# Kernel optimization log

Measured on AMD Instinct MI355X. Metric: run time of the kernel, lower is better.

Reference implementation:

```python
import jax, jax.numpy as jnp
import numpy as np

HEAD_DIM = 64
NUM_FEATURES = 256


def _sample_orf(head_dim, num_features, seed=0):
    """Orthogonal random features with chi(d)-norm row scaling (FAVOR+)."""
    rng = np.random.RandomState(seed)
    blocks = []
    while len(blocks) * head_dim < num_features:
        G = rng.randn(head_dim, head_dim).astype(np.float32)
        Q, _ = np.linalg.qr(G)
        norms = np.linalg.norm(rng.randn(head_dim, head_dim).astype(np.float32), axis=1)
        blocks.append(np.diag(norms) @ Q.T)
    return np.concatenate(blocks, axis=0)[:num_features].astype(np.float32)


def _phi(x, omega, is_query):
    """FAVOR+ positive feature map with max-subtraction stabilization."""
    m = omega.shape[0]
    proj = jnp.einsum('bhnd,md->bhnm', x, omega)          # [B,H,N,M]
    norm = 0.5 * jnp.sum(x * x, axis=-1, keepdims=True)    # [B,H,N,1]
    log_phi = proj - norm
    if is_query:
        log_phi = log_phi - jnp.max(log_phi, axis=-1, keepdims=True)
    else:
        log_phi = log_phi - jnp.max(log_phi)
    return jnp.exp(log_phi) / np.float32(np.sqrt(m)) + 1e-4


def _causal_scan(phi_q, phi_k, v):
    """Causal linear-attention recurrence via lax.scan. States: S[B,H,M,D], z[B,H,M]."""
    B, H, N, M = phi_q.shape
    D = v.shape[-1]
    # seq-first for scan: [N,B,H,*]
    pq = jnp.moveaxis(phi_q, 2, 0)
    pk = jnp.moveaxis(phi_k, 2, 0)
    vt = jnp.moveaxis(v, 2, 0)

    S0 = jnp.zeros((B, H, M, D), dtype=phi_q.dtype)
    z0 = jnp.zeros((B, H, M), dtype=phi_q.dtype)

    def step(carry, xs):
        S, z = carry
        pq_i, pk_i, v_i = xs  # [B,H,M], [B,H,M], [B,H,D]
        S = S + pk_i[..., :, None] * v_i[..., None, :]
        z = z + pk_i
        num = jnp.einsum('bhm,bhmd->bhd', pq_i, S)
        den = jnp.sum(pq_i * z, axis=-1, keepdims=True) + 1e-6
        return (S, z), num / den

    _, out = jax.lax.scan(step, (S0, z0), (pq, pk, vt))  # out: [N,B,H,D]
    return jnp.moveaxis(out, 0, 2)


def setup_inputs() -> dict:
    key = jax.random.key(0)
    k1, k2, k3 = jax.random.split(key, 3)
    B, H, N, D = 2, 16, 4096, HEAD_DIM
    q = jax.random.normal(k1, (B, H, N, D), dtype=jnp.float32)
    k = jax.random.normal(k2, (B, H, N, D), dtype=jnp.float32)
    v = jax.random.normal(k3, (B, H, N, D), dtype=jnp.float32)
    omega = jnp.asarray(_sample_orf(HEAD_DIM, NUM_FEATURES))
    return {"q": q, "k": k, "v": v, "omega": omega}


def reference(q, k, v, omega):
    scale = q.shape[-1] ** (-0.25)
    phi_q = _phi(q * scale, omega, is_query=True)
    phi_k = _phi(k * scale, omega, is_query=False)
    # q_len == kv_len -> causal scan branch (matches original forward)
    out = _causal_scan(phi_q.astype(jnp.float32), phi_k.astype(jnp.float32),
                       v.astype(jnp.float32))
    return out.astype(q.dtype)
```

## Files before the change

kernel.cpp:

```cpp
#include <hip/hip_runtime.h>
#include <cstddef>

#define BH    32
#define NSEQ  4096
#define MFEAT 256
#define CHUNK 128
#define NCH   32
#define SROW  65
#define SPITCH (SROW*256)

#define SCALE 0.35355339059327373f

typedef unsigned int uint_t;
typedef _Float16 half_t;
typedef __attribute__((ext_vector_type(8))) _Float16 half8;
typedef __attribute__((ext_vector_type(4))) float f32x4;

__device__ __forceinline__ f32x4 mfma16(half8 a, half8 b, f32x4 c) {
  return __builtin_amdgcn_mfma_f32_16x16x32_f16(a, b, c, 0, 0, 0);
}
__device__ __forceinline__ uint_t enc_f(float x) {
  uint_t u = __float_as_uint(x);
  return (u & 0x80000000u) ? ~u : (u | 0x80000000u);
}
__device__ __forceinline__ float dec_f(uint_t u) {
  u = (u & 0x80000000u) ? (u ^ 0x80000000u) : ~u;
  return __uint_as_float(u);
}
__device__ __forceinline__ half8 cvt_h8(float4 a, float4 b) {
  half8 h;
  h[0] = (half_t)a.x; h[1] = (half_t)a.y; h[2] = (half_t)a.z; h[3] = (half_t)a.w;
  h[4] = (half_t)b.x; h[5] = (half_t)b.y; h[6] = (half_t)b.z; h[7] = (half_t)b.w;
  return h;
}

__global__ void k_init(uint_t* kmax) { *kmax = enc_f(-__builtin_inff()); }

__global__ __launch_bounds__(256, 2) void k_maxes3(
    const float* __restrict__ q, const float* __restrict__ kx,
    const float* __restrict__ omega, uint_t* __restrict__ kmax,
    half_t* __restrict__ phiQ, half_t* __restrict__ kh,
    float* __restrict__ hnKg)
{
  __shared__ half_t Wl[256 * 72];
  __shared__ float nrm[64];
  __shared__ float red[4];

  const int tid = threadIdx.x;
  const int lane = tid & 63;
  const int w = tid >> 6;
  const int lc = lane & 15, rg = lane >> 4, koff = rg * 8;
  const size_t rowbase = (size_t)blockIdx.x * 64;

  for (int l = tid; l < 4096; l += 256) {
    int m = l >> 4, d4 = (l & 15) * 4;
    float4 o = *(const float4*)(omega + m * 64 + d4);
    half_t* p = &Wl[m * 72 + d4];
    p[0] = (half_t)o.x; p[1] = (half_t)o.y; p[2] = (half_t)o.z; p[3] = (half_t)o.w;
  }
  half8 aq[2], akf[2];
  {
    const float* qp = q + (rowbase + w * 16 + lc) * 64 + koff;
    const float* kp = kx + (rowbase + w * 16 + lc) * 64 + koff;
    float pn = 0.f;
    #pragma unroll
    for (int ks = 0; ks < 2; ks++) {
      float4 a = *(const float4*)(qp + ks * 32);
      float4 b = *(const float4*)(qp + ks * 32 + 4);
      a.x *= SCALE; a.y *= SCALE; a.z *= SCALE; a.w *= SCALE;
      b.x *= SCALE; b.y *= SCALE; b.z *= SCALE; b.w *= SCALE;
      aq[ks] = cvt_h8(a, b);
      float4 c = *(const float4*)(kp + ks * 32);
      float4 d = *(const float4*)(kp + ks * 32 + 4);
      c.x *= SCALE; c.y *= SCALE; c.z *= SCALE; c.w *= SCALE;
      d.x *= SCALE; d.y *= SCALE; d.z *= SCALE; d.w *= SCALE;
      pn += c.x * c.x + c.y * c.y + c.z * c.z + c.w * c.w
          + d.x * d.x + d.y * d.y + d.z * d.z + d.w * d.w;
      akf[ks] = cvt_h8(c, d);
    }
    #pragma unroll
    for (int ks = 0; ks < 2; ks++)
      *(half8*)(kh + (rowbase + w * 16 + lc) * 64 + ks * 32 + koff) = akf[ks];
    pn += __shfl_xor(pn, 16, 64);
    pn += __shfl_xor(pn, 32, 64);
    if (rg == 0) {
      nrm[w * 16 + lc] = 0.5f * pn;
      hnKg[rowbase + w * 16 + lc] = 0.5f * pn;
    }
  }
  __syncthreads();

  {
    f32x4 acc[16];
    #pragma unroll
    for (int ct = 0; ct < 16; ct++) acc[ct] = (f32x4){0.f, 0.f, 0.f, 0.f};
    #pragma unroll
    for (int ks = 0; ks < 2; ks++)
      #pragma unroll
      for (int ct = 0; ct < 16; ct++) {
        half8 b = *(const half8*)&Wl[(ct * 16 + lc) * 72 + ks * 32 + koff];
        acc[ct] = mfma16(akf[ks], b, acc[ct]);
      }
    float hn[4];
    #pragma unroll
    for (int r = 0; r < 4; r++) hn[r] = nrm[w * 16 + rg * 4 + r];
    float bm = -3.4e38f;
    #pragma unroll
    for (int ct = 0; ct < 16; ct++)
      #pragma unroll
      for (int r = 0; r < 4; r++) bm = fmaxf(bm, acc[ct][r] - hn[r]);
    #pragma unroll
    for (int off = 1; off < 64; off <<= 1) bm = fmaxf(bm, __shfl_xor(bm, off, 64));
    if (lane == 0) red[w] = bm;
  }

  f32x4 acc[16];
  #pragma unroll
  for (int ct = 0; ct < 16; ct++) acc[ct] = (f32x4){0.f, 0.f, 0.f, 0.f};
  #pragma unroll
  for (int ks = 0; ks < 2; ks++)
    #pragma unroll
    for (int ct = 0; ct < 16; ct++) {
      half8 b = *(const half8*)&Wl[(ct * 16 + lc) * 72 + ks * 32 + koff];
      acc[ct] = mfma16(aq[ks], b, acc[ct]);
    }
  float rowm[4];
  #pragma unroll
  for (int r = 0; r < 4; r++) {
    float m0 = -3.4e38f;
    #pragma unroll
    for (int ct = 0; ct < 16; ct++) m0 = fmaxf(m0, acc[ct][r]);
    m0 = fmaxf(m0, __shfl_xor(m0, 1, 64));
    m0 = fmaxf(m0, __shfl_xor(m0, 2, 64));
    m0 = fmaxf(m0, __shfl_xor(m0, 4, 64));
    m0 = fmaxf(m0, __shfl_xor(m0, 8, 64));
    rowm[r] = m0;
  }
  #pragma unroll
  for (int ct = 0; ct < 16; ct++)
    #pragma unroll
    for (int r = 0; r < 4; r++)
      acc[ct][r] = __expf(acc[ct][r] - rowm[r]) * 0.0625f + 1e-4f;

  __syncthreads();
  if (tid == 0)
    atomicMax(kmax, enc_f(fmaxf(fmaxf(red[0], red[1]), fmaxf(red[2], red[3]))));

  half_t* st = Wl;
  #pragma unroll
  for (int ct = 0; ct < 16; ct++)
    #pragma unroll
    for (int r = 0; r < 4; r++)
      st[(w * 16 + rg * 4 + r) * 264 + ct * 16 + lc] = (half_t)acc[ct][r];
  __syncthreads();
  #pragma unroll
  for (int e = 0; e < 8; e++) {
    int l = tid + e * 256;
    int row = l >> 5, c = (l & 31) * 8;
    *(half8*)(phiQ + (rowbase + row) * 256 + c) = *(const half8*)&st[row * 264 + c];
  }
}

__global__ __launch_bounds__(256, 2) void k_state3(
    const half_t* __restrict__ kh, const float* __restrict__ v,
    const float* __restrict__ omega, const float* __restrict__ hnKg,
    const uint_t* __restrict__ kmax, half_t* __restrict__ spA,
    half_t* __restrict__ phiKg)
{
  __shared__ half_t WP[256 * 72];
  __shared__ half_t vt[80 * 136];

  const int tid = threadIdx.x;
  const int lane = tid & 63;
  const int w = tid >> 6;
  const int lc = lane & 15, rg = lane >> 4, koff = rg * 8;
  const int wr = w * 32;
  const int blk = blockIdx.x;
  const size_t nbase = (size_t)(blk >> 5) * NSEQ + (size_t)(blk & 31) * CHUNK;
  const float gmaxv = dec_f(*kmax);

  for (int l = tid; l < 4096; l += 256) {
    int m = l >> 4, d4 = (l & 15) * 4;
    float4 o = *(const float4*)(omega + m * 64 + d4);
    half_t* p = &WP[m * 72 + d4];
    p[0] = (half_t)o.x; p[1] = (half_t)o.y; p[2] = (half_t)o.z; p[3] = (half_t)o.w;
  }
  for (int l = tid; l < 2048; l += 256) {
    int j = l >> 4, dq = (l & 15) * 4;
    float4 vv = *(const float4*)(v + (nbase + j) * 64 + dq);
    vt[(dq + 0) * 136 + j] = (half_t)vv.x;
    vt[(dq + 1) * 136 + j] = (half_t)vv.y;
    vt[(dq + 2) * 136 + j] = (half_t)vv.z;
    vt[(dq + 3) * 136 + j] = (half_t)vv.w;
  }
  if (tid < 128) vt[64 * 136 + tid] = (half_t)1.0f;

  half8 ak[2][2];
  float hnr[2][4];
  #pragma unroll
  for (int rt = 0; rt < 2; rt++) {
    const half_t* kp = kh + (nbase + wr + rt * 16 + lc) * 64 + koff;
    ak[rt][0] = *(const half8*)(kp);
    ak[rt][1] = *(const half8*)(kp + 32);
    #pragma unroll
    for (int r = 0; r < 4; r++)
      hnr[rt][r] = hnKg[nbase + wr + rt * 16 + rg * 4 + r];
  }
  __syncthreads();

  f32x4 accP[2][16];
  #pragma unroll
  for (int rt = 0; rt < 2; rt++)
    #pragma unroll
    for (int ct = 0; ct < 16; ct++) accP[rt][ct] = (f32x4){0.f, 0.f, 0.f, 0.f};
  #pragma unroll
  for (int ks = 0; ks < 2; ks++)
    #pragma unroll
    for (int ct = 0; ct < 16; ct++) {
      half8 b = *(const half8*)&WP[(ct * 16 + lc) * 72 + ks * 32 + koff];
      accP[0][ct] = mfma16(ak[0][ks], b, accP[0][ct]);
      accP[1][ct] = mfma16(ak[1][ks], b, accP[1][ct]);
    }
  #pragma unroll
  for (int rt = 0; rt < 2; rt++)
    #pragma unroll
    for (int ct = 0; ct < 16; ct++)
      #pragma unroll
      for (int r = 0; r < 4; r++)
        accP[rt][ct][r] = __expf(accP[rt][ct][r] - hnr[rt][r] - gmaxv) * 0.0625f + 1e-4f;

  half_t* pkT = WP;
  #pragma unroll
  for (int h = 0; h < 2; h++) {
    __syncthreads();
    #pragma unroll
    for (int rt = 0; rt < 2; rt++)
      #pragma unroll
      for (int c8 = 0; c8 < 8; c8++) {
        int ct = h * 8 + c8;
        #pragma unroll
        for (int r = 0; r < 4; r++)
          pkT[(c8 * 16 + lc) * 144 + wr + rt * 16 + rg * 4 + r] = (half_t)accP[rt][ct][r];
      }
    __syncthreads();
    f32x4 acc2[5][2];
    #pragma unroll
    for (int rt = 0; rt < 5; rt++) {
      acc2[rt][0] = (f32x4){0.f, 0.f, 0.f, 0.f};
      acc2[rt][1] = (f32x4){0.f, 0.f, 0.f, 0.f};
    }
    #pragma unroll
    for (int ks = 0; ks < 4; ks++) {
      half8 b0 = *(const half8*)&pkT[((2 * w + 0) * 16 + lc) * 144 + ks * 32 + koff];
      half8 b1 = *(const half8*)&pkT[((2 * w + 1) * 16 + lc) * 144 + ks * 32 + koff];
      #pragma unroll
      for (int rt = 0; rt < 5; rt++) {
        half8 a = *(const half8*)&vt[(rt * 16 + lc) * 136 + ks * 32 + koff];
        acc2[rt][0] = mfma16(a, b0, acc2[rt][0]);
        acc2[rt][1] = mfma16(a, b1, acc2[rt][1]);
      }
    }
    #pragma unroll
    for (int rt = 0; rt < 5; rt++)
      #pragma unroll
      for (int c2 = 0; c2 < 2; c2++)
        #pragma unroll
        for (int r = 0; r < 4; r++) {
          int row = rt * 16 + rg * 4 + r;
          if (row < SROW)
            spA[(size_t)blk * SPITCH + row * 256 + h * 128 + (2 * w + c2) * 16 + lc] =
                (half_t)acc2[rt][c2][r];
        }
  }

  half_t* PhS = WP;
  #pragma unroll
  for (int hh = 0; hh < 2; hh++) {
    __syncthreads();
    #pragma unroll
    for (int rt = 0; rt < 2; rt++)
      #pragma unroll
      for (int c8 = 0; c8 < 8; c8++)
        #pragma unroll
        for (int r = 0; r < 4; r++)
          PhS[(wr + rt * 16 + rg * 4 + r) * 136 + c8 * 16 + lc] =
              (half_t)accP[rt][hh * 8 + c8][r];
    __syncthreads();
    #pragma unroll
    for (int e = 0; e < 8; e++) {
      int l = tid + e * 256;
      int j = l >> 4, c8b = (l & 15) * 8;
      *(half8*)(phiKg + (nbase + j) * 256 + hh * 128 + c8b) =
          *(const half8*)&PhS[j * 136 + c8b];
    }
  }
}

__global__ __launch_bounds__(256) void k_prefix(
    const uint_t* __restrict__ spA, uint_t* __restrict__ spB)
{
  int r = blockIdx.x * 256 + threadIdx.x;
  if (r >= SPITCH / 2) return;
  int bh = blockIdx.y;
  const uint_t* src = spA + (size_t)bh * NCH * (SPITCH / 2) + r;
  uint_t* dst = spB + (size_t)bh * NCH * (SPITCH / 2) + r;
  float r0 = 0.f, r1 = 0.f;
  for (int c = 0; c < NCH; c++) {
    union { uint_t u; half_t h[2]; } cv, ov;
    cv.u = src[(size_t)c * (SPITCH / 2)];
    ov.h[0] = (half_t)r0; ov.h[1] = (half_t)r1;
    dst[(size_t)c * (SPITCH / 2)] = ov.u;
    r0 += (float)cv.h[0];
    r1 += (float)cv.h[1];
  }
}

__global__ __launch_bounds__(512) void k_attn8(
    const half_t* __restrict__ phiQ, const half_t* __restrict__ phiK,
    const float* __restrict__ v, const half_t* __restrict__ spB,
    float* __restrict__ out)
{
  __shared__ half_t sm[18432];
  half_t* PQ  = sm;
  half_t* SST = sm + 8192;
  half_t* AS  = sm;
  half_t* VT  = sm + 8192;

  const int tid = threadIdx.x;
  const int lane = tid & 63;
  const int w = tid >> 6;
  const int lc = lane & 15, rg = lane >> 4, koff = rg * 8;
  const int blk = blockIdx.x;
  const size_t nbase = (size_t)(blk >> 5) * NSEQ + (size_t)(blk & 31) * CHUNK;
  const half_t* spb = spB + (size_t)blk * SPITCH;
  const int swz = (lc & 7) << 3;

  f32x4 accA[8], accO[5];
  #pragma unroll
  for (int it = 0; it < 8; it++) accA[it] = (f32x4){0.f, 0.f, 0.f, 0.f};
  #pragma unroll
  for (int cs = 0; cs < 5; cs++) accO[cs] = (f32x4){0.f, 0.f, 0.f, 0.f};

  for (int mt = 0; mt < 4; mt++) {
    if (mt) __syncthreads();
    #pragma unroll
    for (int e = 0; e < 2; e++) {
      int l = tid + e * 512;
      int ro = l >> 3, c8 = (l & 7) * 8;
      *(half8*)&PQ[ro * 64 + (c8 ^ ((ro & 7) << 3))] =
          *(const half8*)(phiQ + (nbase + ro) * 256 + mt * 64 + c8);
    }
    { int ro = tid >> 3, c8 = (tid & 7) * 8;
      if (tid < 520)
        *(half8*)&SST[ro * 64 + (c8 ^ ((ro & 7) << 3))] =
            *(const half8*)(spb + ro * 256 + mt * 64 + c8); }
    if (tid < 8) { int l = tid + 512; int ro = l >> 3, c8 = (l & 7) * 8;
      *(half8*)&SST[ro * 64 + (c8 ^ ((ro & 7) << 3))] =
          *(const half8*)(spb + ro * 256 + mt * 64 + c8); }
    half8 af0 = *(const half8*)(phiK + (nbase + w * 16 + lc) * 256 + mt * 64 + koff);
    half8 af1 = *(const half8*)(phiK + (nbase + w * 16 + lc) * 256 + mt * 64 + 32 + koff);
    __syncthreads();
    #pragma unroll
    for (int ks2 = 0; ks2 < 64; ks2 += 32) {
      half8 a = ks2 ? af1 : af0;
      int sA = (ks2 + koff) ^ swz;
      half8 bO = *(const half8*)&PQ[(w * 16 + lc) * 64 + sA];
      #pragma unroll
      for (int it = 0; it < 8; it++) {
        half8 b = *(const half8*)&PQ[(it * 16 + lc) * 64 + sA];
        accA[it] = mfma16(a, b, accA[it]);
      }
      #pragma unroll
      for (int cs = 0; cs < 5; cs++) {
        half8 as_ = *(const half8*)&SST[(cs * 16 + lc) * 64 + sA];
        accO[cs] = mfma16(as_, bO, accO[cs]);
      }
    }
  }
  __syncthreads();

  #pragma unroll
  for (int e = 0; e < 4; e++) {
    int l = tid + e * 512;
    int j = l >> 4, dq = (l & 15) * 4;
    float4 vv = *(const float4*)(v + (nbase + j) * 64 + dq);
    VT[(dq + 0) * 128 + (j ^ (((dq + 0) & 7) << 3))] = (half_t)vv.x;
    VT[(dq + 1) * 128 + (j ^ (((dq + 1) & 7) << 3))] = (half_t)vv.y;
    VT[(dq + 2) * 128 + (j ^ (((dq + 2) & 7) << 3))] = (half_t)vv.z;
    VT[(dq + 3) * 128 + (j ^ (((dq + 3) & 7) << 3))] = (half_t)vv.w;
  }
  if (tid < 128) VT[64 * 128 + tid] = (half_t)1.0f;

  #pragma unroll
  for (int h = 0; h < 2; h++) {
    if ((w >> 2) == h) {
      #pragma unroll
      for (int it = 0; it < 8; it++) {
        int i = it * 16 + lc;
        #pragma unroll
        for (int r = 0; r < 4; r++) {
          int j = w * 16 + rg * 4 + r;
          float val = (j <= i) ? accA[it][r] : 0.f;
          AS[i * 64 + ((j - h * 64) ^ ((i & 7) << 3))] = (half_t)val;
        }
      }
    }
    __syncthreads();
    #pragma unroll
    for (int ks2 = 0; ks2 < 64; ks2 += 32) {
      int sj = (ks2 + koff) ^ swz;
      half8 b = *(const half8*)&AS[(w * 16 + lc) * 64 + sj];
      #pragma unroll
      for (int cs = 0; cs < 5; cs++) {
        half8 a = *(const half8*)&VT[(cs * 16 + lc) * 128 + ((h * 64 + ks2 + koff) ^ swz)];
        accO[cs] = mfma16(a, b, accO[cs]);
      }
    }
    __syncthreads();
  }

  float den = __shfl(accO[4][0], lane & 15, 64) + 1e-6f;
  float inv = 1.0f / den;
  float* OS = (float*)sm;
  #pragma unroll
  for (int cs = 0; cs < 4; cs++)
    #pragma unroll
    for (int r = 0; r < 4; r++)
      OS[(w * 16 + lc) * 68 + cs * 16 + rg * 4 + r] = accO[cs][r] * inv;
  __syncthreads();
  #pragma unroll
  for (int e = 0; e < 4; e++) {
    int l = tid + e * 512;
    int row = l >> 4, c4 = (l & 15) * 4;
    *(float4*)(out + (nbase + row) * 64 + c4) = *(const float4*)&OS[row * 68 + c4];
  }
}

extern "C" void kernel_launch(void* const* d_in, const int* in_sizes, int n_in,
                              void* d_out, int out_size, void* d_ws, size_t ws_size,
                              hipStream_t stream) {
  const float* q = (const float*)d_in[0];
  const float* k = (const float*)d_in[1];
  const float* v = (const float*)d_in[2];
  const float* omega = (const float*)d_in[3];
  float* out = (float*)d_out;
  char* ws = (char*)d_ws;

  float*  hnKg = (float*)(ws + 0);
  half_t* kh   = (half_t*)(ws + 524288);
  half_t* spB  = (half_t*)(ws + 524288);
  half_t* phiQ = (half_t*)(ws + 34603008);
  half_t* phiK = (half_t*)(ws + 101711872);
  half_t* spA  = (half_t*)(ws + 168820736);
  uint_t* kmax = (uint_t*)(ws + 202899456);

  k_init<<<1, 1, 0, stream>>>(kmax);
  k_maxes3<<<2048, 256, 0, stream>>>(q, k, omega, kmax, phiQ, kh, hnKg);
  k_state3<<<1024, 256, 0, stream>>>(kh, v, omega, hnKg, kmax, spA, phiK);
  k_prefix<<<dim3(33, 32), 256, 0, stream>>>((const uint_t*)spA, (uint_t*)spB);
  k_attn8<<<1024, 512, 0, stream>>>(phiQ, phiK, v, spB, out);
}
```

Before: 167.2 us.

## Swizzle LDS tiles and recompute fp16 k in state kernel instead of staging

Replaces padded shared-memory layouts (row pitch 72/136/144) with unpadded XOR-swizzled layouts for omega, v-transpose, phiK-transpose and staging tiles. The aim is to avoid bank conflicts while using less LDS. It also drops the fp16 copy of k written by the first kernel; the state kernel now reloads fp32 k, scales it and converts it itself. The phiQ store is split into two half-width passes to fit the smaller buffer. This trades one workspace write and read for an extra fp32 load of k and some added address arithmetic.

```diff
diff --git a/kernel.cpp b/kernel.cpp
--- a/kernel.cpp
+++ b/kernel.cpp
@@ -36,13 +36,12 @@
 
 __global__ void k_init(uint_t* kmax) { *kmax = enc_f(-__builtin_inff()); }
 
-__global__ __launch_bounds__(256, 2) void k_maxes3(
+__global__ __launch_bounds__(256, 2) void k_maxes4(
     const float* __restrict__ q, const float* __restrict__ kx,
     const float* __restrict__ omega, uint_t* __restrict__ kmax,
-    half_t* __restrict__ phiQ, half_t* __restrict__ kh,
-    float* __restrict__ hnKg)
+    half_t* __restrict__ phiQ, float* __restrict__ hnKg)
 {
-  __shared__ half_t Wl[256 * 72];
+  __shared__ half_t Wl[256 * 64];
   __shared__ float nrm[64];
   __shared__ float red[4];
 
@@ -50,13 +49,14 @@
   const int lane = tid & 63;
   const int w = tid >> 6;
   const int lc = lane & 15, rg = lane >> 4, koff = rg * 8;
+  const int swz = (lc & 7) << 3;
   const size_t rowbase = (size_t)blockIdx.x * 64;
 
-  for (int l = tid; l < 4096; l += 256) {
-    int m = l >> 4, d4 = (l & 15) * 4;
-    float4 o = *(const float4*)(omega + m * 64 + d4);
-    half_t* p = &Wl[m * 72 + d4];
-    p[0] = (half_t)o.x; p[1] = (half_t)o.y; p[2] = (half_t)o.z; p[3] = (half_t)o.w;
+  for (int l = tid; l < 2048; l += 256) {
+    int m = l >> 3, d8 = (l & 7) * 8;
+    float4 a = *(const float4*)(omega + m * 64 + d8);
+    float4 b = *(const float4*)(omega + m * 64 + d8 + 4);
+    *(half8*)&Wl[m * 64 + (d8 ^ ((m & 7) << 3))] = cvt_h8(a, b);
   }
   half8 aq[2], akf[2];
   {
@@ -78,9 +78,6 @@
           + d.x * d.x + d.y * d.y + d.z * d.z + d.w * d.w;
       akf[ks] = cvt_h8(c, d);
     }
-    #pragma unroll
-    for (int ks = 0; ks < 2; ks++)
-      *(half8*)(kh + (rowbase + w * 16 + lc) * 64 + ks * 32 + koff) = akf[ks];
     pn += __shfl_xor(pn, 16, 64);
     pn += __shfl_xor(pn, 32, 64);
     if (rg == 0) {
@@ -91,15 +88,15 @@
   __syncthreads();
 
   {
-    f32x4 acc[16];
-    #pragma unroll
-    for (int ct = 0; ct < 16; ct++) acc[ct] = (f32x4){0.f, 0.f, 0.f, 0.f};
+    f32x4 acck[16];
+    #pragma unroll
+    for (int ct = 0; ct < 16; ct++) acck[ct] = (f32x4){0.f, 0.f, 0.f, 0.f};
     #pragma unroll
     for (int ks = 0; ks < 2; ks++)
       #pragma unroll
       for (int ct = 0; ct < 16; ct++) {
-        half8 b = *(const half8*)&Wl[(ct * 16 + lc) * 72 + ks * 32 + koff];
-        acc[ct] = mfma16(akf[ks], b, acc[ct]);
+        half8 b = *(const half8*)&Wl[(ct * 16 + lc) * 64 + ((ks * 32 + koff) ^ swz)];
+        acck[ct] = mfma16(akf[ks], b, acck[ct]);
       }
     float hn[4];
     #pragma unroll
@@ -108,7 +105,7 @@
     #pragma unroll
     for (int ct = 0; ct < 16; ct++)
       #pragma unroll
-      for (int r = 0; r < 4; r++) bm = fmaxf(bm, acc[ct][r] - hn[r]);
+      for (int r = 0; r < 4; r++) bm = fmaxf(bm, acck[ct][r] - hn[r]);
     #pragma unroll
     for (int off = 1; off < 64; off <<= 1) bm = fmaxf(bm, __shfl_xor(bm, off, 64));
     if (lane == 0) red[w] = bm;
@@ -121,7 +118,7 @@
   for (int ks = 0; ks < 2; ks++)
     #pragma unroll
     for (int ct = 0; ct < 16; ct++) {
-      half8 b = *(const half8*)&Wl[(ct * 16 + lc) * 72 + ks * 32 + koff];
+      half8 b = *(const half8*)&Wl[(ct * 16 + lc) * 64 + ((ks * 32 + koff) ^ swz)];
       acc[ct] = mfma16(aq[ks], b, acc[ct]);
     }
   float rowm[4];
@@ -148,60 +145,72 @@
 
   half_t* st = Wl;
   #pragma unroll
-  for (int ct = 0; ct < 16; ct++)
-    #pragma unroll
-    for (int r = 0; r < 4; r++)
-      st[(w * 16 + rg * 4 + r) * 264 + ct * 16 + lc] = (half_t)acc[ct][r];
-  __syncthreads();
-  #pragma unroll
-  for (int e = 0; e < 8; e++) {
-    int l = tid + e * 256;
-    int row = l >> 5, c = (l & 31) * 8;
-    *(half8*)(phiQ + (rowbase + row) * 256 + c) = *(const half8*)&st[row * 264 + c];
-  }
-}
-
-__global__ __launch_bounds__(256, 2) void k_state3(
-    const half_t* __restrict__ kh, const float* __restrict__ v,
+  for (int hh = 0; hh < 2; hh++) {
+    if (hh) __syncthreads();
+    #pragma unroll
+    for (int c8 = 0; c8 < 8; c8++)
+      #pragma unroll
+      for (int r = 0; r < 4; r++)
+        st[(w * 16 + rg * 4 + r) * 136 + c8 * 16 + lc] = (half_t)acc[hh * 8 + c8][r];
+    __syncthreads();
+    #pragma unroll
+    for (int e = 0; e < 4; e++) {
+      int l = tid + e * 256;
+      int row = l >> 4, c = (l & 15) * 8;
+      *(half8*)(phiQ + (rowbase + row) * 256 + hh * 128 + c) =
+          *(const half8*)&st[row * 136 + c];
+    }
+  }
+}
+
+__global__ __launch_bounds__(256, 2) void k_state4(
+    const float* __restrict__ kx, const float* __restrict__ v,
     const float* __restrict__ omega, const float* __restrict__ hnKg,
     const uint_t* __restrict__ kmax, half_t* __restrict__ spA,
     half_t* __restrict__ phiKg)
 {
-  __shared__ half_t WP[256 * 72];
-  __shared__ half_t vt[80 * 136];
+  __shared__ half_t WP[256 * 64];
+  __shared__ half_t vt[80 * 128];
 
   const int tid = threadIdx.x;
   const int lane = tid & 63;
   const int w = tid >> 6;
   const int lc = lane & 15, rg = lane >> 4, koff = rg * 8;
   const int wr = w * 32;
+  const int swz = (lc & 7) << 3;
   const int blk = blockIdx.x;
   const size_t nbase = (size_t)(blk >> 5) * NSEQ + (size_t)(blk & 31) * CHUNK;
   const float gmaxv = dec_f(*kmax);
 
-  for (int l = tid; l < 4096; l += 256) {
-    int m = l >> 4, d4 = (l & 15) * 4;
-    float4 o = *(const float4*)(omega + m * 64 + d4);
-    half_t* p = &WP[m * 72 + d4];
-    p[0] = (half_t)o.x; p[1] = (half_t)o.y; p[2] = (half_t)o.z; p[3] = (half_t)o.w;
+  for (int l = tid; l < 2048; l += 256) {
+    int m = l >> 3, d8 = (l & 7) * 8;
+    float4 a = *(const float4*)(omega + m * 64 + d8);
+    float4 b = *(const float4*)(omega + m * 64 + d8 + 4);
+    *(half8*)&WP[m * 64 + (d8 ^ ((m & 7) << 3))] = cvt_h8(a, b);
   }
   for (int l = tid; l < 2048; l += 256) {
     int j = l >> 4, dq = (l & 15) * 4;
     float4 vv = *(const float4*)(v + (nbase + j) * 64 + dq);
-    vt[(dq + 0) * 136 + j] = (half_t)vv.x;
-    vt[(dq + 1) * 136 + j] = (half_t)vv.y;
-    vt[(dq + 2) * 136 + j] = (half_t)vv.z;
-    vt[(dq + 3) * 136 + j] = (half_t)vv.w;
-  }
-  if (tid < 128) vt[64 * 136 + tid] = (half_t)1.0f;
+    vt[(dq + 0) * 128 + (j ^ (((dq + 0) & 7) << 3))] = (half_t)vv.x;
+    vt[(dq + 1) * 128 + (j ^ (((dq + 1) & 7) << 3))] = (half_t)vv.y;
+    vt[(dq + 2) * 128 + (j ^ (((dq + 2) & 7) << 3))] = (half_t)vv.z;
+    vt[(dq + 3) * 128 + (j ^ (((dq + 3) & 7) << 3))] = (half_t)vv.w;
+  }
+  if (tid < 128) vt[64 * 128 + tid] = (half_t)1.0f;
 
   half8 ak[2][2];
   float hnr[2][4];
   #pragma unroll
   for (int rt = 0; rt < 2; rt++) {
-    const half_t* kp = kh + (nbase + wr + rt * 16 + lc) * 64 + koff;
-    ak[rt][0] = *(const half8*)(kp);
-    ak[rt][1] = *(const half8*)(kp + 32);
+    const float* kp = kx + (nbase + wr + rt * 16 + lc) * 64 + koff;
+    #pragma unroll
+    for (int ks = 0; ks < 2; ks++) {
+      float4 a = *(const float4*)(kp + ks * 32);
+      float4 b = *(const float4*)(kp + ks * 32 + 4);
+      a.x *= SCALE; a.y *= SCALE; a.z *= SCALE; a.w *= SCALE;
+      b.x *= SCALE; b.y *= SCALE; b.z *= SCALE; b.w *= SCALE;
+      ak[rt][ks] = cvt_h8(a, b);
+    }
     #pragma unroll
     for (int r = 0; r < 4; r++)
       hnr[rt][r] = hnKg[nbase + wr + rt * 16 + rg * 4 + r];
@@ -217,7 +226,7 @@
   for (int ks = 0; ks < 2; ks++)
     #pragma unroll
     for (int ct = 0; ct < 16; ct++) {
-      half8 b = *(const half8*)&WP[(ct * 16 + lc) * 72 + ks * 32 + koff];
+      half8 b = *(const half8*)&WP[(ct * 16 + lc) * 64 + ((ks * 32 + koff) ^ swz)];
       accP[0][ct] = mfma16(ak[0][ks], b, accP[0][ct]);
       accP[1][ct] = mfma16(ak[1][ks], b, accP[1][ct]);
     }
@@ -237,10 +246,13 @@
     for (int rt = 0; rt < 2; rt++)
       #pragma unroll
       for (int c8 = 0; c8 < 8; c8++) {
+        int m = c8 * 16 + lc;
         int ct = h * 8 + c8;
         #pragma unroll
-        for (int r = 0; r < 4; r++)
-          pkT[(c8 * 16 + lc) * 144 + wr + rt * 16 + rg * 4 + r] = (half_t)accP[rt][ct][r];
+        for (int r = 0; r < 4; r++) {
+          int j = wr + rt * 16 + rg * 4 + r;
+          pkT[m * 128 + (j ^ ((m & 7) << 3))] = (half_t)accP[rt][ct][r];
+        }
       }
     __syncthreads();
     f32x4 acc2[5][2];
@@ -251,11 +263,11 @@
     }
     #pragma unroll
     for (int ks = 0; ks < 4; ks++) {
-      half8 b0 = *(const half8*)&pkT[((2 * w + 0) * 16 + lc) * 144 + ks * 32 + koff];
-      half8 b1 = *(const half8*)&pkT[((2 * w + 1) * 16 + lc) * 144 + ks * 32 + koff];
+      half8 b0 = *(const half8*)&pkT[((2 * w + 0) * 16 + lc) * 128 + ((ks * 32 + koff) ^ swz)];
+      half8 b1 = *(const half8*)&pkT[((2 * w + 1) * 16 + lc) * 128 + ((ks * 32 + koff) ^ swz)];
       #pragma unroll
       for (int rt = 0; rt < 5; rt++) {
-        half8 a = *(const half8*)&vt[(rt * 16 + lc) * 136 + ks * 32 + koff];
+        half8 a = *(const half8*)&vt[(rt * 16 + lc) * 128 + ((ks * 32 + koff) ^ swz)];
         acc2[rt][0] = mfma16(a, b0, acc2[rt][0]);
         acc2[rt][1] = mfma16(a, b1, acc2[rt][1]);
       }
@@ -282,16 +294,18 @@
       #pragma unroll
       for (int c8 = 0; c8 < 8; c8++)
         #pragma unroll
-        for (int r = 0; r < 4; r++)
-          PhS[(wr + rt * 16 + rg * 4 + r) * 136 + c8 * 16 + lc] =
+        for (int r = 0; r < 4; r++) {
+          int j = wr + rt * 16 + rg * 4 + r;
+          PhS[j * 128 + ((c8 * 16 + lc) ^ ((j & 7) << 3))] =
               (half_t)accP[rt][hh * 8 + c8][r];
+        }
     __syncthreads();
     #pragma unroll
     for (int e = 0; e < 8; e++) {
       int l = tid + e * 256;
       int j = l >> 4, c8b = (l & 15) * 8;
       *(half8*)(phiKg + (nbase + j) * 256 + hh * 128 + c8b) =
-          *(const half8*)&PhS[j * 136 + c8b];
+          *(const half8*)&PhS[j * 128 + (c8b ^ ((j & 7) << 3))];
     }
   }
 }
@@ -447,7 +461,6 @@
   char* ws = (char*)d_ws;
 
   float*  hnKg = (float*)(ws + 0);
-  half_t* kh   = (half_t*)(ws + 524288);
   half_t* spB  = (half_t*)(ws + 524288);
   half_t* phiQ = (half_t*)(ws + 34603008);
   half_t* phiK = (half_t*)(ws + 101711872);
@@ -455,8 +468,8 @@
   uint_t* kmax = (uint_t*)(ws + 202899456);
 
   k_init<<<1, 1, 0, stream>>>(kmax);
-  k_maxes3<<<2048, 256, 0, stream>>>(q, k, omega, kmax, phiQ, kh, hnKg);
-  k_state3<<<1024, 256, 0, stream>>>(kh, v, omega, hnKg, kmax, spA, phiK);
+  k_maxes4<<<2048, 256, 0, stream>>>(q, k, omega, kmax, phiQ, hnKg);
+  k_state4<<<1024, 256, 0, stream>>>(k, v, omega, hnKg, kmax, spA, phiK);
   k_prefix<<<dim3(33, 32), 256, 0, stream>>>((const uint_t*)spA, (uint_t*)spB);
   k_attn8<<<1024, 512, 0, stream>>>(phiQ, phiK, v, spB, out);
 }
```

Measured after the change: 154.6 us. 1.08x faster.
